# Performance work log

Hardware: AMD Instinct MI355X
Metric: run time of the kernel (lower is better)

## Reference

```python
import jax, jax.numpy as jnp
import numpy as np

N_NODES = 50000
N_EDGES = 800000
N_PAIRS = 200000
IN_DIM = 128
HID = 64
OUT_DIM = 1


def _gat_layer(x, W, a_l, a_r, src, dst, n_nodes):
    # Single-head GAT (DGL-style): z = xW; attention logits from learned
    # left/right vectors; softmax over incoming edges of each dst node.
    z = x @ W                                   # [N, H]
    el = z @ a_l                                # [N]
    er = z @ a_r                                # [N]
    e = jax.nn.leaky_relu(el[src] + er[dst], 0.2)   # [E]
    emax = jax.ops.segment_max(e, dst, num_segments=n_nodes)  # [N]
    ex = jnp.exp(e - emax[dst])                 # [E], stable softmax numerator
    denom = jax.ops.segment_sum(ex, dst, num_segments=n_nodes)  # [N]
    msg = ex[:, None] * z[src]                  # [E, H]
    agg = jax.ops.segment_sum(msg, dst, num_segments=n_nodes)   # [N, H]
    return agg / jnp.maximum(denom, 1e-9)[:, None]


def setup_inputs() -> dict:
    key = jax.random.key(0)
    ks = jax.random.split(key, 10)
    feat = jax.random.normal(ks[0], (N_NODES, IN_DIM), dtype=jnp.float32)
    src = jax.random.randint(ks[1], (N_EDGES,), 0, N_NODES, dtype=jnp.int32)
    dst = jax.random.randint(ks[2], (N_EDGES,), 0, N_NODES, dtype=jnp.int32)
    # query pairs: take existing edges so the has_edges_between mask is true
    pair_src = src[:N_PAIRS]
    pair_dst = dst[:N_PAIRS]
    s1 = 1.0 / np.sqrt(IN_DIM)
    s2 = 1.0 / np.sqrt(HID)
    W1 = jax.random.normal(ks[3], (IN_DIM, HID), dtype=jnp.float32) * s1
    al1 = jax.random.normal(ks[4], (HID,), dtype=jnp.float32) * s2
    ar1 = jax.random.normal(ks[5], (HID,), dtype=jnp.float32) * s2
    W2 = jax.random.normal(ks[6], (HID, HID), dtype=jnp.float32) * s2
    al2 = jax.random.normal(ks[7], (HID,), dtype=jnp.float32) * s2
    ar2 = jax.random.normal(ks[8], (HID,), dtype=jnp.float32) * s2
    Wc = jax.random.normal(ks[9], (2 * HID, OUT_DIM), dtype=jnp.float32) * s2
    bc = jnp.zeros((OUT_DIM,), dtype=jnp.float32)
    return {"feat": feat, "W1": W1, "al1": al1, "ar1": ar1,
            "W2": W2, "al2": al2, "ar2": ar2, "Wc": Wc, "bc": bc,
            "src": src, "dst": dst, "pair_src": pair_src, "pair_dst": pair_dst}


def reference(feat, W1, al1, ar1, W2, al2, ar2, Wc, bc, src, dst, pair_src, pair_dst):
    src = src.astype(jnp.int32)
    dst = dst.astype(jnp.int32)
    # two hetero GAT layers (single ntype -> mean aggregate is identity) + ReLU
    h = jax.nn.relu(_gat_layer(feat, W1, al1, ar1, src, dst, N_NODES))
    h = jax.nn.relu(_gat_layer(h, W2, al2, ar2, src, dst, N_NODES))
    # has_edges_between(pair_src, pair_dst): membership test via sorted edge keys
    ekeys = src.astype(jnp.int64) * N_NODES + dst.astype(jnp.int64)
    skeys = jnp.sort(ekeys)
    pkeys = pair_src.astype(jnp.int64) * N_NODES + pair_dst.astype(jnp.int64)
    idx = jnp.clip(jnp.searchsorted(skeys, pkeys), 0, N_EDGES - 1)
    mask = (skeys[idx] == pkeys)                 # [P] bool
    # gather endpoint embeddings, concat, classify, sigmoid; invalid rows -> 0
    hs = h[pair_src]                             # [P, H]
    hd = h[pair_dst]                             # [P, H]
    h_pair = jnp.concatenate([hs, hd], axis=1)   # [P, 2H]
    out = jax.nn.sigmoid(h_pair @ Wc + bc)       # [P, OUT]
    return out * mask[:, None].astype(out.dtype)
```

## Files before the change

kernel.cpp:

```cpp
#include <hip/hip_runtime.h>
#include <cstdint>

#define N_NODES 50000
#define N_EDGES 800000
#define N_PAIRS 200000
#define IN_DIM 128
#define HID 64
#define N_WAVES_GEMM (N_NODES / 16)
#define NBIN 196
#define NCH 320
#define CHUNK ((N_EDGES + NCH - 1) / NCH)
#define MHIST (NBIN * NCH)
#define SBG ((MHIST + 255) / 256)
#define MB_GEMM ((N_WAVES_GEMM + 3) / 4)
#define NODE_BLOCKS ((N_NODES + 3) / 4)
#define MEMBER_BLOCKS (N_PAIRS / 32)

typedef __attribute__((ext_vector_type(8))) short bf16x8;
typedef __attribute__((ext_vector_type(4))) float f32x4;

__device__ __forceinline__ unsigned short bf16_rne(float f) {
    unsigned u = __float_as_uint(f);
    unsigned t = u + 0x7FFFu + ((u >> 16) & 1u);
    return (unsigned short)(t >> 16);
}
__device__ __forceinline__ void bf2f(unsigned u, float& a, float& b) {
    a = __uint_as_float(u << 16);
    b = __uint_as_float(u & 0xFFFF0000u);
}

__global__ __launch_bounds__(256) void hist_prep(
    const int* __restrict__ dst, int* __restrict__ histHi,
    const float* __restrict__ W1, const float* __restrict__ W2,
    unsigned short* __restrict__ w1hi, unsigned short* __restrict__ w1lo,
    unsigned short* __restrict__ w2hi, unsigned short* __restrict__ w2lo)
{
    const int t = threadIdx.x, b = blockIdx.x;
    if (b < NCH) {
        __shared__ int hist[256];
        hist[t] = 0; __syncthreads();
        const int beg = b * CHUNK, end = min(beg + CHUNK, N_EDGES);
        for (int e = beg + t; e < end; e += 256) atomicAdd(&hist[dst[e] >> 8], 1);
        __syncthreads();
        if (t < NBIN) histHi[t * NCH + b] = hist[t];
    } else {
        int tid = (b - NCH) * 256 + t;
        if (tid < 8192) {
            int jj = tid & 7, lane = (tid >> 3) & 63, tt = (tid >> 9) & 3, ks = tid >> 11;
            int k = ks * 32 + (lane >> 4) * 8 + jj;
            int n = tt * 16 + (lane & 15);
            float f = W1[k * HID + n];
            unsigned short hi = bf16_rne(f);
            float fhi = __uint_as_float(((unsigned)hi) << 16);
            w1hi[tid] = hi;
            w1lo[tid] = bf16_rne(f - fhi);
        }
        if (tid < 4096) {
            int jj = tid & 7, lane = (tid >> 3) & 63, tt = (tid >> 9) & 3, ks = tid >> 11;
            int k = ks * 32 + (lane >> 4) * 8 + jj;
            int n = tt * 16 + (lane & 15);
            float f = W2[k * HID + n];
            unsigned short hi = bf16_rne(f);
            float fhi = __uint_as_float(((unsigned)hi) << 16);
            w2hi[tid] = hi;
            w2lo[tid] = bf16_rne(f - fhi);
        }
    }
}

__global__ __launch_bounds__(256) void scan1g(
    int* __restrict__ histHi, int* __restrict__ bsums)
{
    __shared__ int sh[256];
    const int t = threadIdx.x;
    const int i = blockIdx.x * 256 + t;
    int v = (i < MHIST) ? histHi[i] : 0;
    sh[t] = v; __syncthreads();
    #pragma unroll
    for (int off = 1; off < 256; off <<= 1) {
        int x = sh[t];
        int a = (t >= off) ? sh[t - off] : 0;
        __syncthreads();
        sh[t] = x + a;
        __syncthreads();
    }
    if (i < MHIST) histHi[i] = sh[t] - v;
    if (t == 255) bsums[blockIdx.x] = sh[255];
}

__device__ __forceinline__ void scan_bsums(const int* __restrict__ bsums,
                                           int* sh, int* exb, int t)
{
    int v = (t < SBG) ? bsums[t] : 0;
    sh[t] = v; __syncthreads();
    #pragma unroll
    for (int off = 1; off < 256; off <<= 1) {
        int x = sh[t];
        int a = (t >= off) ? sh[t - off] : 0;
        __syncthreads();
        sh[t] = x + a;
        __syncthreads();
    }
    exb[t] = sh[t] - v;
    __syncthreads();
}

__device__ __forceinline__ void gemm1_body(
    int wave, int lane,
    const float* __restrict__ x,
    const unsigned short* __restrict__ whi, const unsigned short* __restrict__ wlo,
    const float* __restrict__ al, const float* __restrict__ ar,
    unsigned short* __restrict__ z, float* __restrict__ el, float* __restrict__ er)
{
    const int i0 = wave * 16;
    const int m = lane & 15, quad = lane >> 4;
    f32x4 acc[4] = {{0.f,0.f,0.f,0.f},{0.f,0.f,0.f,0.f},{0.f,0.f,0.f,0.f},{0.f,0.f,0.f,0.f}};
    const float* xrow = x + (size_t)(i0 + m) * IN_DIM;

    #pragma unroll 1
    for (int ks = 0; ks < 4; ++ks) {
        const float4 xv0 = *(const float4*)&xrow[ks * 32 + quad * 8];
        const float4 xv1 = *(const float4*)&xrow[ks * 32 + quad * 8 + 4];
        float xs[8] = {xv0.x, xv0.y, xv0.z, xv0.w, xv1.x, xv1.y, xv1.z, xv1.w};
        bf16x8 ahi, alo;
        #pragma unroll
        for (int jj = 0; jj < 8; ++jj) {
            unsigned short hb = bf16_rne(xs[jj]);
            float fhi = __uint_as_float(((unsigned)hb) << 16);
            ahi[jj] = (short)hb;
            alo[jj] = (short)bf16_rne(xs[jj] - fhi);
        }
        #pragma unroll
        for (int t = 0; t < 4; ++t) {
            const bf16x8 bhi = *(const bf16x8*)&whi[(((ks * 4 + t) * 64) + lane) * 8];
            const bf16x8 blo = *(const bf16x8*)&wlo[(((ks * 4 + t) * 64) + lane) * 8];
            acc[t] = __builtin_amdgcn_mfma_f32_16x16x32_bf16(ahi, bhi, acc[t], 0, 0, 0);
            acc[t] = __builtin_amdgcn_mfma_f32_16x16x32_bf16(ahi, blo, acc[t], 0, 0, 0);
            acc[t] = __builtin_amdgcn_mfma_f32_16x16x32_bf16(alo, bhi, acc[t], 0, 0, 0);
        }
    }
    #pragma unroll
    for (int r = 0; r < 4; ++r) {
        const int row = quad * 4 + r;
        float se = 0.f, sr = 0.f;
        #pragma unroll
        for (int t = 0; t < 4; ++t) {
            float v = acc[t][r];
            z[(size_t)(i0 + row) * HID + t * 16 + m] = bf16_rne(v);
            se = fmaf(v, al[t * 16 + m], se);
            sr = fmaf(v, ar[t * 16 + m], sr);
        }
        #pragma unroll
        for (int off = 1; off < 16; off <<= 1) {
            se += __shfl_xor(se, off, 64);
            sr += __shfl_xor(sr, off, 64);
        }
        if (m == 0) { el[i0 + row] = se; er[i0 + row] = sr; }
    }
}

__global__ __launch_bounds__(256) void scatter_gemm1(
    const int* __restrict__ src, const int* __restrict__ dst,
    const int* __restrict__ histEx, const int* __restrict__ bsums,
    unsigned* __restrict__ pairs,
    const float* __restrict__ x,
    const unsigned short* __restrict__ whi, const unsigned short* __restrict__ wlo,
    const float* __restrict__ al, const float* __restrict__ ar,
    unsigned short* __restrict__ z, float* __restrict__ el, float* __restrict__ er)
{
    const int b = blockIdx.x;
    if (b < NCH) {
        __shared__ int sh[256], exb[256], base[256];
        const int t = threadIdx.y * 64 + threadIdx.x;
        scan_bsums(bsums, sh, exb, t);
        if (t < NBIN) {
            int idx = t * NCH + b;
            base[t] = histEx[idx] + exb[idx >> 8];
        }
        __syncthreads();
        const int beg = b * CHUNK, end = min(beg + CHUNK, N_EDGES);
        for (int e = beg + t; e < end; e += 256) {
            int s = src[e], d = dst[e];
            int pos = atomicAdd(&base[d >> 8], 1);
            pairs[pos] = ((unsigned)s << 16) | (unsigned)d;
        }
    } else {
        const int wave = (b - NCH) * 4 + threadIdx.y;
        if (wave < N_WAVES_GEMM)
            gemm1_body(wave, threadIdx.x, x, whi, wlo, al, ar, z, el, er);
    }
}

__global__ __launch_bounds__(256) void seg_sort(
    const unsigned* __restrict__ pairs, const int* __restrict__ histEx,
    const int* __restrict__ bsums,
    int* __restrict__ row_start, unsigned short* __restrict__ csr_src)
{
    __shared__ int sh[256], exb[256], hist[256], sc[256], offs[256];
    const int t = threadIdx.x, b = blockIdx.x;
    scan_bsums(bsums, sh, exb, t);
    const int i0 = b * NCH;
    const int segStart = histEx[i0] + exb[i0 >> 8];
    int segEnd = N_EDGES;
    if (b < NBIN - 1) {
        const int i1 = (b + 1) * NCH;
        segEnd = histEx[i1] + exb[i1 >> 8];
    }
    hist[t] = 0; __syncthreads();
    for (int i = segStart + t; i < segEnd; i += 256)
        atomicAdd(&hist[pairs[i] & 255], 1);
    __syncthreads();
    int v = hist[t]; sc[t] = v; __syncthreads();
    #pragma unroll
    for (int off = 1; off < 256; off <<= 1) {
        int x = sc[t];
        int a = (t >= off) ? sc[t - off] : 0;
        __syncthreads();
        sc[t] = x + a;
        __syncthreads();
    }
    const int excl = sc[t] - v;
    offs[t] = segStart + excl;
    const int node = b * 256 + t;
    if (node <= N_NODES) row_start[node] = segStart + excl;
    __syncthreads();
    for (int i = segStart + t; i < segEnd; i += 256) {
        unsigned p = pairs[i];
        int pos = atomicAdd(&offs[p & 255], 1);
        csr_src[pos] = (unsigned short)(p >> 16);
    }
}

template <bool LAST>
__device__ __forceinline__ void agg_body(
    int i, int lane,
    const int* __restrict__ row_start, const unsigned short* __restrict__ csr_src,
    const float* __restrict__ el, const float* __restrict__ er,
    const unsigned short* __restrict__ z, unsigned short* __restrict__ hdst,
    const float* __restrict__ Wc, float* __restrict__ as, float* __restrict__ ad)
{
    const int rb = row_start[i], re = row_start[i + 1];
    const float er_i = er[i];
    const int es = lane >> 3;
    const int fl = lane & 7;

    float acc[8] = {0.f,0.f,0.f,0.f,0.f,0.f,0.f,0.f};
    float den = 0.f;

    int eA = rb + es;        bool vA = eA < re;
    int eB = eA + 8;         bool vB = eB < re;
    int sA = vA ? (int)csr_src[eA] : 0;
    int sB = vB ? (int)csr_src[eB] : 0;
    float elA = el[sA];
    uint4 zA = ((const uint4*)(z + (size_t)sA * HID))[fl];

    for (int e0 = rb; e0 < re; e0 += 8) {
        const int eC = e0 + 16 + es;
        const bool vC = eC < re;
        const int sC = vC ? (int)csr_src[eC] : 0;
        const float elB = el[sB];
        const uint4 zB = ((const uint4*)(z + (size_t)sB * HID))[fl];

        float x = elA + er_i;
        float lr = x > 0.f ? x : 0.2f * x;
        float ex = vA ? __expf(lr) : 0.f;
        float z0, z1, z2, z3, z4, z5, z6, z7;
        bf2f(zA.x, z0, z1); bf2f(zA.y, z2, z3);
        bf2f(zA.z, z4, z5); bf2f(zA.w, z6, z7);
        acc[0] = fmaf(ex, z0, acc[0]); acc[1] = fmaf(ex, z1, acc[1]);
        acc[2] = fmaf(ex, z2, acc[2]); acc[3] = fmaf(ex, z3, acc[3]);
        acc[4] = fmaf(ex, z4, acc[4]); acc[5] = fmaf(ex, z5, acc[5]);
        acc[6] = fmaf(ex, z6, acc[6]); acc[7] = fmaf(ex, z7, acc[7]);
        den += ex;

        sA = sB; vA = vB; elA = elB; zA = zB;
        sB = sC; vB = vC;
    }
    #pragma unroll
    for (int off = 8; off < 64; off <<= 1) {
        #pragma unroll
        for (int q = 0; q < 8; ++q) acc[q] += __shfl_xor(acc[q], off, 64);
        den += __shfl_xor(den, off, 64);
    }
    if (es == 0) {
        float inv = 1.f / fmaxf(den, 1e-9f);
        float hv[8];
        #pragma unroll
        for (int q = 0; q < 8; ++q) hv[q] = fmaxf(acc[q] * inv, 0.f);
        if (LAST) {
            float ps = 0.f, pd = 0.f;
            #pragma unroll
            for (int q = 0; q < 8; ++q) {
                ps = fmaf(hv[q], Wc[fl * 8 + q], ps);
                pd = fmaf(hv[q], Wc[HID + fl * 8 + q], pd);
            }
            #pragma unroll
            for (int off = 1; off < 8; off <<= 1) {
                ps += __shfl_xor(ps, off, 64);
                pd += __shfl_xor(pd, off, 64);
            }
            if (fl == 0) { as[i] = ps; ad[i] = pd; }
        } else {
            unsigned short o[8];
            #pragma unroll
            for (int q = 0; q < 8; ++q) o[q] = bf16_rne(hv[q]);
            uint4 pk;
            pk.x = (unsigned)o[0] | ((unsigned)o[1] << 16);
            pk.y = (unsigned)o[2] | ((unsigned)o[3] << 16);
            pk.z = (unsigned)o[4] | ((unsigned)o[5] << 16);
            pk.w = (unsigned)o[6] | ((unsigned)o[7] << 16);
            ((uint4*)hdst)[fl] = pk;
        }
    }
}

__global__ __launch_bounds__(256) void agg1_gemm2_member(
    const int* __restrict__ row_start, const unsigned short* __restrict__ csr_src,
    const float* __restrict__ el1, const float* __restrict__ er1,
    const unsigned short* __restrict__ z1,
    const unsigned short* __restrict__ whi, const unsigned short* __restrict__ wlo,
    const float* __restrict__ al, const float* __restrict__ ar,
    unsigned short* __restrict__ z2, float* __restrict__ el2, float* __restrict__ er2,
    const int* __restrict__ ps, const int* __restrict__ pd, int* __restrict__ found)
{
    const int b = blockIdx.x, lane = threadIdx.x, ty = threadIdx.y;
    if (b < N_WAVES_GEMM) {
        __shared__ __align__(16) unsigned short ht[16][72];
        const int i0 = b * 16;
        #pragma unroll 1
        for (int c = 0; c < 4; ++c) {
            const int r = ty * 4 + c;
            agg_body<false>(i0 + r, lane, row_start, csr_src, el1, er1, z1,
                            &ht[r][0], nullptr, nullptr, nullptr);
        }
        __syncthreads();
        if (ty == 0) {
            const int m = lane & 15, quad = lane >> 4;
            f32x4 acc[4] = {{0.f,0.f,0.f,0.f},{0.f,0.f,0.f,0.f},
                            {0.f,0.f,0.f,0.f},{0.f,0.f,0.f,0.f}};
            const unsigned short* xrow = &ht[m][0];
            #pragma unroll 1
            for (int ks = 0; ks < 2; ++ks) {
                const bf16x8 aa = *(const bf16x8*)&xrow[ks * 32 + quad * 8];
                #pragma unroll
                for (int tt = 0; tt < 4; ++tt) {
                    const bf16x8 bhi = *(const bf16x8*)&whi[(((ks * 4 + tt) * 64) + lane) * 8];
                    const bf16x8 blo = *(const bf16x8*)&wlo[(((ks * 4 + tt) * 64) + lane) * 8];
                    acc[tt] = __builtin_amdgcn_mfma_f32_16x16x32_bf16(aa, bhi, acc[tt], 0, 0, 0);
                    acc[tt] = __builtin_amdgcn_mfma_f32_16x16x32_bf16(aa, blo, acc[tt], 0, 0, 0);
                }
            }
            #pragma unroll
            for (int r = 0; r < 4; ++r) {
                const int row = quad * 4 + r;
                float se = 0.f, sr = 0.f;
                #pragma unroll
                for (int tt = 0; tt < 4; ++tt) {
                    float v = acc[tt][r];
                    z2[(size_t)(i0 + row) * HID + tt * 16 + m] = bf16_rne(v);
                    se = fmaf(v, al[tt * 16 + m], se);
                    sr = fmaf(v, ar[tt * 16 + m], sr);
                }
                #pragma unroll
                for (int off = 1; off < 16; off <<= 1) {
                    se += __shfl_xor(se, off, 64);
                    sr += __shfl_xor(sr, off, 64);
                }
                if (m == 0) { el2[i0 + row] = se; er2[i0 + row] = sr; }
            }
        }
    } else {
        const int r8 = lane & 7, g = lane >> 3;
        const int p = (b - N_WAVES_GEMM) * 32 + ty * 8 + g;
        const int s = ps[p], d = pd[p];
        const int rb = row_start[d], re = row_start[d + 1];
        int f = 0;
        for (int e = rb + r8; e < re; e += 8) f |= ((int)csr_src[e] == s) ? 1 : 0;
        #pragma unroll
        for (int off = 1; off < 8; off <<= 1) f |= __shfl_xor(f, off, 64);
        if (r8 == 0) found[p] = f;
    }
}

__global__ __launch_bounds__(256) void agg2(
    const int* __restrict__ row_start, const unsigned short* __restrict__ csr_src,
    const float* __restrict__ el, const float* __restrict__ er,
    const unsigned short* __restrict__ z, const float* __restrict__ Wc,
    float* __restrict__ as, float* __restrict__ ad)
{
    const int i = blockIdx.x * 4 + threadIdx.y;
    if (i < N_NODES)
        agg_body<true>(i, threadIdx.x, row_start, csr_src, el, er, z,
                       nullptr, Wc, as, ad);
}

__global__ __launch_bounds__(256) void pair_tiny(
    const int* __restrict__ ps, const int* __restrict__ pd,
    const float* __restrict__ as, const float* __restrict__ ad,
    const float* __restrict__ bc, const int* __restrict__ found,
    float* __restrict__ out)
{
    const int p = blockIdx.x * 256 + threadIdx.x;
    if (p >= N_PAIRS) return;
    float v = as[ps[p]] + ad[pd[p]] + bc[0];
    float sg = 1.f / (1.f + __expf(-v));
    out[p] = found[p] ? sg : 0.f;
}

extern "C" void kernel_launch(void* const* d_in, const int* in_sizes, int n_in,
                              void* d_out, int out_size, void* d_ws, size_t ws_size,
                              hipStream_t stream)
{
    const float* feat = (const float*)d_in[0];
    const float* W1   = (const float*)d_in[1];
    const float* al1  = (const float*)d_in[2];
    const float* ar1  = (const float*)d_in[3];
    const float* W2   = (const float*)d_in[4];
    const float* al2  = (const float*)d_in[5];
    const float* ar2  = (const float*)d_in[6];
    const float* Wc   = (const float*)d_in[7];
    const float* bc   = (const float*)d_in[8];
    const int* src    = (const int*)d_in[9];
    const int* dst    = (const int*)d_in[10];
    const int* psrc   = (const int*)d_in[11];
    const int* pdst   = (const int*)d_in[12];
    float* out = (float*)d_out;

    char* ws = (char*)d_ws;
    unsigned short* z  = (unsigned short*)ws;  ws += (size_t)N_NODES * HID * 2;
    unsigned short* z2 = (unsigned short*)ws;  ws += (size_t)N_NODES * HID * 2;
    float* el = (float*)ws;               ws += (size_t)N_NODES * 4;
    float* er = (float*)ws;               ws += (size_t)N_NODES * 4;
    float* as = (float*)ws;               ws += (size_t)N_NODES * 4;
    float* ad = (float*)ws;               ws += (size_t)N_NODES * 4;
    float* el2 = (float*)ws;              ws += (size_t)N_NODES * 4;
    float* er2 = (float*)ws;              ws += (size_t)N_NODES * 4;
    int* row_start = (int*)ws;            ws += (size_t)(N_NODES + 1) * 4;
    int* histHi = (int*)ws;               ws += (size_t)MHIST * 4;
    int* bsumsA = (int*)ws;               ws += (size_t)(SBG + 1) * 4;
    int* found = (int*)ws;                ws += (size_t)N_PAIRS * 4;
    ws = (char*)(((uintptr_t)ws + 255) & ~(uintptr_t)255);
    unsigned* pairs = (unsigned*)ws;      ws += (size_t)N_EDGES * 4;
    unsigned short* csr_src = (unsigned short*)ws;  ws += (size_t)N_EDGES * 2;
    ws = (char*)(((uintptr_t)ws + 255) & ~(uintptr_t)255);
    unsigned short* w1hi = (unsigned short*)ws;  ws += 8192 * 2;
    unsigned short* w1lo = (unsigned short*)ws;  ws += 8192 * 2;
    unsigned short* w2hi = (unsigned short*)ws;  ws += 4096 * 2;
    unsigned short* w2lo = (unsigned short*)ws;  ws += 4096 * 2;

    dim3 b64x4(64, 4);

    hist_prep<<<NCH + 32, 256, 0, stream>>>(dst, histHi, W1, W2, w1hi, w1lo, w2hi, w2lo);
    scan1g<<<SBG, 256, 0, stream>>>(histHi, bsumsA);
    scatter_gemm1<<<NCH + MB_GEMM, b64x4, 0, stream>>>(src, dst, histHi, bsumsA, pairs,
        feat, w1hi, w1lo, al1, ar1, z, el, er);
    seg_sort<<<NBIN, 256, 0, stream>>>(pairs, histHi, bsumsA, row_start, csr_src);
    agg1_gemm2_member<<<N_WAVES_GEMM + MEMBER_BLOCKS, b64x4, 0, stream>>>(
        row_start, csr_src, el, er, z, w2hi, w2lo, al2, ar2,
        z2, el2, er2, psrc, pdst, found);
    agg2<<<NODE_BLOCKS, b64x4, 0, stream>>>(row_start, csr_src, el2, er2, z2, Wc, as, ad);
    pair_tiny<<<(N_PAIRS + 255) / 256, 256, 0, stream>>>(psrc, pdst, as, ad, bc, found, out);
}
```

Before: 182.0 us.

## Replace global histogram scan with atomic bin reservation; prefetch GEMM input rows

Each histogram block now reserves its offsets within each bin through a global atomicAdd on a 256-entry bin cursor. The separate scan1g kernel and the large per-chunk histogram scan are removed; consumers only scan the 256 bin totals. A memset is added to clear the cursor. The ordering of edges within a bin becomes nondeterministic, which the following per-bin sort handles. The GEMM1 loop also software-prefetches the next K-slice of x to hide load latency.

```diff
diff --git a/kernel.cpp b/kernel.cpp
--- a/kernel.cpp
+++ b/kernel.cpp
@@ -10,8 +10,6 @@
 #define NBIN 196
 #define NCH 320
 #define CHUNK ((N_EDGES + NCH - 1) / NCH)
-#define MHIST (NBIN * NCH)
-#define SBG ((MHIST + 255) / 256)
 #define MB_GEMM ((N_WAVES_GEMM + 3) / 4)
 #define NODE_BLOCKS ((N_NODES + 3) / 4)
 #define MEMBER_BLOCKS (N_PAIRS / 32)
@@ -29,8 +27,25 @@
     b = __uint_as_float(u & 0xFFFF0000u);
 }
 
+__device__ __forceinline__ void scan_bins(const int* __restrict__ binCursor,
+                                          int* sh, int* exb, int t)
+{
+    int v = binCursor[t];
+    sh[t] = v; __syncthreads();
+    #pragma unroll
+    for (int off = 1; off < 256; off <<= 1) {
+        int x = sh[t];
+        int a = (t >= off) ? sh[t - off] : 0;
+        __syncthreads();
+        sh[t] = x + a;
+        __syncthreads();
+    }
+    exb[t] = sh[t] - v;
+    __syncthreads();
+}
+
 __global__ __launch_bounds__(256) void hist_prep(
-    const int* __restrict__ dst, int* __restrict__ histHi,
+    const int* __restrict__ dst, int* __restrict__ binCursor, int* __restrict__ resv,
     const float* __restrict__ W1, const float* __restrict__ W2,
     unsigned short* __restrict__ w1hi, unsigned short* __restrict__ w1lo,
     unsigned short* __restrict__ w2hi, unsigned short* __restrict__ w2lo)
@@ -42,7 +57,7 @@
         const int beg = b * CHUNK, end = min(beg + CHUNK, N_EDGES);
         for (int e = beg + t; e < end; e += 256) atomicAdd(&hist[dst[e] >> 8], 1);
         __syncthreads();
-        if (t < NBIN) histHi[t * NCH + b] = hist[t];
+        resv[b * 256 + t] = atomicAdd(&binCursor[t], hist[t]);
     } else {
         int tid = (b - NCH) * 256 + t;
         if (tid < 8192) {
@@ -68,43 +83,6 @@
     }
 }
 
-__global__ __launch_bounds__(256) void scan1g(
-    int* __restrict__ histHi, int* __restrict__ bsums)
-{
-    __shared__ int sh[256];
-    const int t = threadIdx.x;
-    const int i = blockIdx.x * 256 + t;
-    int v = (i < MHIST) ? histHi[i] : 0;
-    sh[t] = v; __syncthreads();
-    #pragma unroll
-    for (int off = 1; off < 256; off <<= 1) {
-        int x = sh[t];
-        int a = (t >= off) ? sh[t - off] : 0;
-        __syncthreads();
-        sh[t] = x + a;
-        __syncthreads();
-    }
-    if (i < MHIST) histHi[i] = sh[t] - v;
-    if (t == 255) bsums[blockIdx.x] = sh[255];
-}
-
-__device__ __forceinline__ void scan_bsums(const int* __restrict__ bsums,
-                                           int* sh, int* exb, int t)
-{
-    int v = (t < SBG) ? bsums[t] : 0;
-    sh[t] = v; __syncthreads();
-    #pragma unroll
-    for (int off = 1; off < 256; off <<= 1) {
-        int x = sh[t];
-        int a = (t >= off) ? sh[t - off] : 0;
-        __syncthreads();
-        sh[t] = x + a;
-        __syncthreads();
-    }
-    exb[t] = sh[t] - v;
-    __syncthreads();
-}
-
 __device__ __forceinline__ void gemm1_body(
     int wave, int lane,
     const float* __restrict__ x,
@@ -117,11 +95,16 @@
     f32x4 acc[4] = {{0.f,0.f,0.f,0.f},{0.f,0.f,0.f,0.f},{0.f,0.f,0.f,0.f},{0.f,0.f,0.f,0.f}};
     const float* xrow = x + (size_t)(i0 + m) * IN_DIM;
 
+    float4 c0 = *(const float4*)&xrow[quad * 8];
+    float4 c1 = *(const float4*)&xrow[quad * 8 + 4];
     #pragma unroll 1
     for (int ks = 0; ks < 4; ++ks) {
-        const float4 xv0 = *(const float4*)&xrow[ks * 32 + quad * 8];
-        const float4 xv1 = *(const float4*)&xrow[ks * 32 + quad * 8 + 4];
-        float xs[8] = {xv0.x, xv0.y, xv0.z, xv0.w, xv1.x, xv1.y, xv1.z, xv1.w};
+        float4 n0, n1;
+        if (ks < 3) {
+            n0 = *(const float4*)&xrow[(ks + 1) * 32 + quad * 8];
+            n1 = *(const float4*)&xrow[(ks + 1) * 32 + quad * 8 + 4];
+        }
+        float xs[8] = {c0.x, c0.y, c0.z, c0.w, c1.x, c1.y, c1.z, c1.w};
         bf16x8 ahi, alo;
         #pragma unroll
         for (int jj = 0; jj < 8; ++jj) {
@@ -138,6 +121,7 @@
             acc[t] = __builtin_amdgcn_mfma_f32_16x16x32_bf16(ahi, blo, acc[t], 0, 0, 0);
             acc[t] = __builtin_amdgcn_mfma_f32_16x16x32_bf16(alo, bhi, acc[t], 0, 0, 0);
         }
+        c0 = n0; c1 = n1;
     }
     #pragma unroll
     for (int r = 0; r < 4; ++r) {
@@ -161,7 +145,7 @@
 
 __global__ __launch_bounds__(256) void scatter_gemm1(
     const int* __restrict__ src, const int* __restrict__ dst,
-    const int* __restrict__ histEx, const int* __restrict__ bsums,
+    const int* __restrict__ binCursor, const int* __restrict__ resv,
     unsigned* __restrict__ pairs,
     const float* __restrict__ x,
     const unsigned short* __restrict__ whi, const unsigned short* __restrict__ wlo,
@@ -172,11 +156,8 @@
     if (b < NCH) {
         __shared__ int sh[256], exb[256], base[256];
         const int t = threadIdx.y * 64 + threadIdx.x;
-        scan_bsums(bsums, sh, exb, t);
-        if (t < NBIN) {
-            int idx = t * NCH + b;
-            base[t] = histEx[idx] + exb[idx >> 8];
-        }
+        scan_bins(binCursor, sh, exb, t);
+        base[t] = exb[t] + resv[b * 256 + t];
         __syncthreads();
         const int beg = b * CHUNK, end = min(beg + CHUNK, N_EDGES);
         for (int e = beg + t; e < end; e += 256) {
@@ -192,20 +173,14 @@
 }
 
 __global__ __launch_bounds__(256) void seg_sort(
-    const unsigned* __restrict__ pairs, const int* __restrict__ histEx,
-    const int* __restrict__ bsums,
+    const unsigned* __restrict__ pairs, const int* __restrict__ binCursor,
     int* __restrict__ row_start, unsigned short* __restrict__ csr_src)
 {
     __shared__ int sh[256], exb[256], hist[256], sc[256], offs[256];
     const int t = threadIdx.x, b = blockIdx.x;
-    scan_bsums(bsums, sh, exb, t);
-    const int i0 = b * NCH;
-    const int segStart = histEx[i0] + exb[i0 >> 8];
-    int segEnd = N_EDGES;
-    if (b < NBIN - 1) {
-        const int i1 = (b + 1) * NCH;
-        segEnd = histEx[i1] + exb[i1 >> 8];
-    }
+    scan_bins(binCursor, sh, exb, t);
+    const int segStart = exb[b];
+    const int segEnd = (b < 255) ? exb[b + 1] : N_EDGES;
     hist[t] = 0; __syncthreads();
     for (int i = segStart + t; i < segEnd; i += 256)
         atomicAdd(&hist[pairs[i] & 255], 1);
@@ -436,8 +411,8 @@
     float* el2 = (float*)ws;              ws += (size_t)N_NODES * 4;
     float* er2 = (float*)ws;              ws += (size_t)N_NODES * 4;
     int* row_start = (int*)ws;            ws += (size_t)(N_NODES + 1) * 4;
-    int* histHi = (int*)ws;               ws += (size_t)MHIST * 4;
-    int* bsumsA = (int*)ws;               ws += (size_t)(SBG + 1) * 4;
+    int* binCursor = (int*)ws;            ws += 256 * 4;
+    int* resv = (int*)ws;                 ws += (size_t)NCH * 256 * 4;
     int* found = (int*)ws;                ws += (size_t)N_PAIRS * 4;
     ws = (char*)(((uintptr_t)ws + 255) & ~(uintptr_t)255);
     unsigned* pairs = (unsigned*)ws;      ws += (size_t)N_EDGES * 4;
@@ -450,11 +425,12 @@
 
     dim3 b64x4(64, 4);
 
-    hist_prep<<<NCH + 32, 256, 0, stream>>>(dst, histHi, W1, W2, w1hi, w1lo, w2hi, w2lo);
-    scan1g<<<SBG, 256, 0, stream>>>(histHi, bsumsA);
-    scatter_gemm1<<<NCH + MB_GEMM, b64x4, 0, stream>>>(src, dst, histHi, bsumsA, pairs,
-        feat, w1hi, w1lo, al1, ar1, z, el, er);
-    seg_sort<<<NBIN, 256, 0, stream>>>(pairs, histHi, bsumsA, row_start, csr_src);
+    hipMemsetAsync(binCursor, 0, 256 * sizeof(int), stream);
+    hist_prep<<<NCH + 32, 256, 0, stream>>>(dst, binCursor, resv,
+        W1, W2, w1hi, w1lo, w2hi, w2lo);
+    scatter_gemm1<<<NCH + MB_GEMM, b64x4, 0, stream>>>(src, dst, binCursor, resv,
+        pairs, feat, w1hi, w1lo, al1, ar1, z, el, er);
+    seg_sort<<<NBIN, 256, 0, stream>>>(pairs, binCursor, row_start, csr_src);
     agg1_gemm2_member<<<N_WAVES_GEMM + MEMBER_BLOCKS, b64x4, 0, stream>>>(
         row_start, csr_src, el, er, z, w2hi, w2lo, al2, ar2,
         z2, el2, er2, psrc, pdst, found);
```

New measurement: 193.9 us. 6.6% more time.
